# Optimization experiments

Hardware: AMD Instinct MI355X
Metric: run time of the kernel (lower is better)

The kernel has to match this reference:

```python
import jax, jax.numpy as jnp
from jax import lax
import numpy as np

N, L, LQ, D, AF, K = 4096, 512, 32, 30, 10, 4  # n_sents, sent_len, q_len, embed_dim, extra feats, conv size


def setup_inputs() -> dict:
    key = jax.random.key(0)
    ks = jax.random.split(key, 10)
    fan_conv = 1.0 / np.sqrt(D * K)
    fan_lin = 1.0 / np.sqrt(AF + 3)
    return {
        "sents_embeds": jax.random.normal(ks[0], (N, L, D), jnp.float32),
        "question_embeds": jax.random.normal(ks[1], (LQ, D), jnp.float32),
        "sents_gaf": jax.random.normal(ks[2], (N, AF), jnp.float32),
        "sents_labels": jax.random.randint(ks[3], (N,), 0, 2),
        "conv1_w": jax.random.uniform(ks[4], (D, D, K), jnp.float32, -fan_conv, fan_conv),
        "conv1_b": jax.random.uniform(ks[5], (D,), jnp.float32, -fan_conv, fan_conv),
        "conv2_w": jax.random.uniform(ks[6], (D, D, K), jnp.float32, -fan_conv, fan_conv),
        "conv2_b": jax.random.uniform(ks[7], (D,), jnp.float32, -fan_conv, fan_conv),
        "lin_w": jax.random.uniform(ks[8], (2, AF + 3), jnp.float32, -fan_lin, fan_lin),
        "lin_b": jax.random.uniform(ks[9], (2,), jnp.float32, -fan_lin, fan_lin),
    }


def _conv1d(x, w, b):
    # x: [B, C, T], w: [O, I, K] (torch layout), padding = K-1 both sides (as torch padding=K-1)
    y = lax.conv_general_dilated(x, w, window_strides=(1,), padding=[(K - 1, K - 1)],
                                 dimension_numbers=("NCW", "OIW", "NCW"))
    return y + b[None, :, None]


def _window_pool(x):
    # avg_pool1d(kernel=K, stride=1) over last axis
    return lax.reduce_window(x, 0.0, lax.add, (1, 1, K), (1, 1, 1), "VALID") / K


def _gpool(x):
    # global average pool over last axis -> [B, C]
    return jnp.mean(x, axis=-1)


def _cos(a, b):
    # a: [N, D] or [D], b: [N, D] or [D] -> cosine similarity, broadcasting
    num = jnp.sum(a * b, axis=-1)
    den = jnp.linalg.norm(a, axis=-1) * jnp.linalg.norm(b, axis=-1)
    return num / den


def _forward(sents_embeds, question_embeds, sents_gaf, sents_labels,
             conv1_w, conv1_b, conv2_w, conv2_b, lin_w, lin_b):
    q = question_embeds.T[None]                # [1, D, LQ]
    s = jnp.transpose(sents_embeds, (0, 2, 1))  # [N, D, L]

    # question side (identical every loop iteration in the original)
    q_raw = _gpool(q)[0]                        # [D]
    q1c = _conv1d(q, conv1_w, conv1_b)          # [1, D, LQ+3]
    q1g = _gpool(q1c)[0]                        # [D]
    q1w = _window_pool(q1c)                     # [1, D, LQ]
    q2c = _conv1d(q1w, conv2_w, conv2_b)        # [1, D, LQ+3]
    q2g = _gpool(q2c)[0]                        # [D]

    # sentence side, batched over N
    s_raw = _gpool(s)                           # [N, D]
    s1c = _conv1d(s, conv1_w, conv1_b)          # [N, D, L+3]
    s1g = _gpool(s1c)                           # [N, D]
    s1w = _window_pool(s1c)                     # [N, D, L]
    s2c = _conv1d(s1w, conv2_w, conv2_b)        # [N, D, L+3]
    s2g = _gpool(s2c)                           # [N, D]

    # sim1: original overwrites quest_global_pool in the loop, so i=0 uses the raw
    # question pool and i>0 use the conv2-level question pool from the prior iter.
    sim1_raw = _cos(q_raw[None], s_raw)         # [N]
    sim1_q2 = _cos(q2g[None], s_raw)            # [N]
    sim1 = jnp.where(jnp.arange(s_raw.shape[0]) == 0, sim1_raw, sim1_q2)
    sim2 = _cos(q1g[None], s1g)                 # [N]
    sim3 = _cos(q2g[None], s2g)                 # [N]

    mlp_in = jnp.concatenate([sim1[:, None], sim2[:, None], sim3[:, None], sents_gaf], axis=-1)  # [N, 13]
    logits = mlp_in @ lin_w.T + lin_b           # [N, 2]
    logp = jax.nn.log_softmax(logits, axis=-1)
    cost = -jnp.mean(jnp.take_along_axis(logp, sents_labels[:, None], axis=-1)[:, 0])
    emit = jax.nn.softmax(logp, axis=-1)[:, 1]  # softmax applied to log_softmax, as in original
    return cost, emit


def reference(sents_embeds, question_embeds, sents_gaf, sents_labels,
              conv1_w, conv1_b, conv2_w, conv2_b, lin_w, lin_b):
    return _forward(sents_embeds, question_embeds, sents_gaf, sents_labels,
                    conv1_w, conv1_b, conv2_w, conv2_b, lin_w, lin_b)
```

## Files before the change

### kernel.cpp

```cpp
#include <hip/hip_runtime.h>
#include <math.h>

#define NS 4096
#define LL 512
#define LQS 32
#define DD 30
#define AFN 10
#define KW 4

enum {
  QRAW = 0,
  Q1G  = 30,
  Q2G  = 60,
  NRM  = 90,
  WS1  = 96,
  WS2  = 996,
  OA0  = 1896,
  OA1  = 2796,
  OA2  = 3696,
  OB0  = 4596,
  OB1  = 5496,
  OB2  = 6396,
  WTOT = 7296
};

__global__ __launch_bounds__(256) void prep_kernel(
    const float* __restrict__ qe,
    const float* __restrict__ w1,
    const float* __restrict__ b1,
    const float* __restrict__ w2,
    const float* __restrict__ b2,
    float* __restrict__ ws,
    float* __restrict__ out)
{
    __shared__ float w1s[DD * DD * KW];
    __shared__ float w2s[DD * DD * KW];
    __shared__ float qT[DD][LQS];
    __shared__ float q1c[DD][LQS + 3];
    __shared__ float q1w[DD][LQS];
    __shared__ float q2c[DD][LQS + 3];
    __shared__ float qpool[3][DD];
    const int tid = threadIdx.x;

    for (int f = tid; f < DD * DD * KW; f += 256) {
        w1s[f] = w1[f];
        w2s[f] = w2[f];
    }
    for (int f = tid; f < LQS * DD; f += 256) {
        qT[f % DD][f / DD] = qe[f];
    }
    __syncthreads();

    for (int idx = tid; idx < DD * (LQS + 3); idx += 256) {
        int o = idx / (LQS + 3), t = idx % (LQS + 3);
        float acc = b1[o];
        for (int i = 0; i < DD; i++) {
            const float* w = w1s + (o * DD + i) * KW;
            #pragma unroll
            for (int k = 0; k < KW; k++) {
                int j = t + k - 3;
                if (j >= 0 && j < LQS) acc += qT[i][j] * w[k];
            }
        }
        q1c[o][t] = acc;
    }
    __syncthreads();

    for (int idx = tid; idx < DD * LQS; idx += 256) {
        int o = idx / LQS, t = idx % LQS;
        q1w[o][t] = 0.25f * (q1c[o][t] + q1c[o][t + 1] + q1c[o][t + 2] + q1c[o][t + 3]);
    }
    __syncthreads();

    for (int idx = tid; idx < DD * (LQS + 3); idx += 256) {
        int o = idx / (LQS + 3), t = idx % (LQS + 3);
        float acc = b2[o];
        for (int i = 0; i < DD; i++) {
            const float* w = w2s + (o * DD + i) * KW;
            #pragma unroll
            for (int k = 0; k < KW; k++) {
                int j = t + k - 3;
                if (j >= 0 && j < LQS) acc += q1w[i][j] * w[k];
            }
        }
        q2c[o][t] = acc;
    }
    __syncthreads();

    if (tid < DD) {
        float a = 0.f;
        for (int t = 0; t < LQS; t++) a += qT[tid][t];
        qpool[0][tid] = a * (1.0f / LQS);
        float g1 = 0.f;
        for (int t = 0; t < LQS + 3; t++) g1 += q1c[tid][t];
        qpool[1][tid] = g1 * (1.0f / (LQS + 3));
        float g2 = 0.f;
        for (int t = 0; t < LQS + 3; t++) g2 += q2c[tid][t];
        qpool[2][tid] = g2 * (1.0f / (LQS + 3));
        ws[QRAW + tid] = qpool[0][tid];
        ws[Q1G + tid]  = qpool[1][tid];
        ws[Q2G + tid]  = qpool[2][tid];
    }
    __syncthreads();
    if (tid < 3) {
        float s = 0.f;
        for (int i = 0; i < DD; i++) { float v = qpool[tid][i]; s += v * v; }
        ws[NRM + tid] = sqrtf(s);
    }
    if (tid >= 3 && tid < 6) ws[NRM + tid] = 0.f;
    if (tid == 0) out[0] = 0.0f;

    for (int idx = tid; idx < DD * DD; idx += 256) {
        int o = idx / DD, i = idx % DD;
        int tr = i * DD + o;
        const float* w = w1s + idx * KW;
        float a = w[0], b = w[1], c = w[2], d = w[3];
        ws[WS1 + tr] = a + b + c + d;
        ws[OA0 + tr] = 3.f * d + 2.f * c + b;
        ws[OA1 + tr] = 2.f * d + c;
        ws[OA2 + tr] = d;
        ws[OB0 + tr] = a;
        ws[OB1 + tr] = b + 2.f * a;
        ws[OB2 + tr] = c + 2.f * b + 3.f * a;
        const float* v = w2s + idx * KW;
        ws[WS2 + tr] = v[0] + v[1] + v[2] + v[3];
    }
}

__global__ __launch_bounds__(256) void stream_post_kernel(
    const float* __restrict__ se,
    const float* __restrict__ gaf,
    const int*   __restrict__ labels,
    const float* __restrict__ b1,
    const float* __restrict__ b2,
    const float* __restrict__ linw,
    const float* __restrict__ linb,
    const float* __restrict__ ws,
    float* __restrict__ out)
{
    const int n   = blockIdx.x;
    const int tid = threadIdx.x;
    const float* base = se + (size_t)n * (LL * DD);

    __shared__ float tabs[WTOT];
    __shared__ float partial[960];
    __shared__ float bnd[6][DD];

    {
        const float4* src = (const float4*)ws;
        float4* dst = (float4*)tabs;
        #pragma unroll
        for (int f = tid; f < WTOT / 4; f += 256) dst[f] = src[f];
    }
    if (tid < 240) {
        const float4* p = (const float4*)base + tid;
        float sx = 0.f, sy = 0.f, sz = 0.f, sw = 0.f;
        #pragma unroll
        for (int it = 0; it < 16; it++) {
            float4 v = p[it * 240];
            sx += v.x; sy += v.y; sz += v.z; sw += v.w;
        }
        partial[4 * tid + 0] = sx;
        partial[4 * tid + 1] = sy;
        partial[4 * tid + 2] = sz;
        partial[4 * tid + 3] = sw;
    }
    if (tid < 180) {
        int r = tid / DD, c = tid % DD;
        int j = (r < 3) ? r : (LL - 6 + r);
        bnd[r][c] = base[j * DD + c];
    }
    __syncthreads();

    if (tid < 64) {
        const int lane = tid;
        const bool act = (lane < DD);
        const int  ic  = act ? lane : 0;

        float S_i = 0.f;
        #pragma unroll
        for (int m = 0; m < 32; m++) S_i += partial[ic + DD * m];

        float e0r = bnd[0][ic], e1r = bnd[1][ic], e2r = bnd[2][ic];
        float e3r = bnd[3][ic], e4r = bnd[4][ic], e5r = bnd[5][ic];
        float bb1 = b1[ic], bb2 = b2[ic];

        float dotS = 0.f, edge = 0.f;
        #pragma unroll 6
        for (int ii = 0; ii < DD; ii++) {
            float s   = __shfl(S_i, ii, 64);
            float b0  = __shfl(e0r, ii, 64);
            float b1v = __shfl(e1r, ii, 64);
            float b2v = __shfl(e2r, ii, 64);
            float b3v = __shfl(e3r, ii, 64);
            float b4v = __shfl(e4r, ii, 64);
            float b5v = __shfl(e5r, ii, 64);
            const int t = ii * DD + ic;
            dotS += s * tabs[WS1 + t];
            edge += b0 * tabs[OA0 + t] + b1v * tabs[OA1 + t] + b2v * tabs[OA2 + t]
                  + b3v * tabs[OB0 + t] + b4v * tabs[OB1 + t] + b5v * tabs[OB2 + t];
        }
        float s1g = dotS * (1.0f / (LL + 3)) + bb1;
        float Tv  = dotS + (float)LL * bb1 - 0.25f * edge;

        float dot2 = 0.f;
        #pragma unroll 6
        for (int ii = 0; ii < DD; ii++) {
            float tv = __shfl(Tv, ii, 64);
            dot2 += tv * tabs[WS2 + ii * DD + ic];
        }
        float s2g = dot2 * (1.0f / (LL + 3)) + bb2;

        float qv = (n == 0) ? tabs[QRAW + ic] : tabs[Q2G + ic];
        float q1 = tabs[Q1G + ic];
        float q2 = tabs[Q2G + ic];
        float p0 = act ? qv * S_i : 0.f;
        float p1 = act ? S_i * S_i : 0.f;
        float p2 = act ? q1 * s1g : 0.f;
        float p3 = act ? s1g * s1g : 0.f;
        float p4 = act ? q2 * s2g : 0.f;
        float p5 = act ? s2g * s2g : 0.f;
        #pragma unroll
        for (int off = 32; off >= 1; off >>= 1) {
            p0 += __shfl_xor(p0, off, 64);
            p1 += __shfl_xor(p1, off, 64);
            p2 += __shfl_xor(p2, off, 64);
            p3 += __shfl_xor(p3, off, 64);
            p4 += __shfl_xor(p4, off, 64);
            p5 += __shfl_xor(p5, off, 64);
        }

        if (lane == 0) {
            float nq = (n == 0) ? tabs[NRM + 0] : tabs[NRM + 2];
            float sim1 = p0 / (nq * sqrtf(p1));
            float sim2 = p2 / (tabs[NRM + 1] * sqrtf(p3));
            float sim3 = p4 / (tabs[NRM + 2] * sqrtf(p5));

            float in[3 + AFN];
            in[0] = sim1; in[1] = sim2; in[2] = sim3;
            const float* g = gaf + (size_t)n * AFN;
            #pragma unroll
            for (int j = 0; j < AFN; j++) in[3 + j] = g[j];

            float l0 = linb[0], l1 = linb[1];
            #pragma unroll
            for (int j = 0; j < 3 + AFN; j++) {
                l0 += in[j] * linw[j];
                l1 += in[j] * linw[(3 + AFN) + j];
            }
            float m = fmaxf(l0, l1);
            float lse = m + logf(expf(l0 - m) + expf(l1 - m));
            float lp0 = l0 - lse, lp1 = l1 - lse;
            float mm = fmaxf(lp0, lp1);
            float ee0 = expf(lp0 - mm), ee1 = expf(lp1 - mm);
            out[1 + n] = ee1 / (ee0 + ee1);
            int lab = labels[n];
            float lp = (lab == 0) ? lp0 : lp1;
            atomicAdd(&out[0], -lp * (1.0f / NS));
        }
    }
}

extern "C" void kernel_launch(void* const* d_in, const int* in_sizes, int n_in,
                              void* d_out, int out_size, void* d_ws, size_t ws_size,
                              hipStream_t stream)
{
    (void)in_sizes; (void)n_in; (void)out_size; (void)ws_size;
    const float* se  = (const float*)d_in[0];
    const float* qe  = (const float*)d_in[1];
    const float* gaf = (const float*)d_in[2];
    const int*   lab = (const int*)d_in[3];
    const float* w1  = (const float*)d_in[4];
    const float* b1  = (const float*)d_in[5];
    const float* w2  = (const float*)d_in[6];
    const float* b2  = (const float*)d_in[7];
    const float* lw  = (const float*)d_in[8];
    const float* lb  = (const float*)d_in[9];
    float* out = (float*)d_out;
    float* ws  = (float*)d_ws;

    hipLaunchKernelGGL(prep_kernel, dim3(1), dim3(256), 0, stream,
                       qe, w1, b1, w2, b2, ws, out);
    hipLaunchKernelGGL(stream_post_kernel, dim3(NS), dim3(256), 0, stream,
                       se, gaf, lab, b1, b2, lw, lb, ws, out);
}
```

Baseline: 425.4 us.

## Process four sentences per block with double-buffered prefetch of next sentence

```diff
diff --git a/kernel.cpp b/kernel.cpp
--- a/kernel.cpp
+++ b/kernel.cpp
@@ -7,6 +7,8 @@
 #define DD 30
 #define AFN 10
 #define KW 4
+#define SPB 4
+#define NBLK (NS / SPB)
 
 enum {
   QRAW = 0,
@@ -138,126 +140,175 @@
     const float* __restrict__ ws,
     float* __restrict__ out)
 {
-    const int n   = blockIdx.x;
     const int tid = threadIdx.x;
-    const float* base = se + (size_t)n * (LL * DD);
+    const int n0  = blockIdx.x * SPB;
 
     __shared__ float tabs[WTOT];
-    __shared__ float partial[960];
-    __shared__ float bnd[6][DD];
+    __shared__ float partial[2][960];
+    __shared__ float bnd[2][6][DD];
 
     {
         const float4* src = (const float4*)ws;
         float4* dst = (float4*)tabs;
-        #pragma unroll
         for (int f = tid; f < WTOT / 4; f += 256) dst[f] = src[f];
     }
-    if (tid < 240) {
-        const float4* p = (const float4*)base + tid;
-        float sx = 0.f, sy = 0.f, sz = 0.f, sw = 0.f;
-        #pragma unroll
-        for (int it = 0; it < 16; it++) {
-            float4 v = p[it * 240];
-            sx += v.x; sy += v.y; sz += v.z; sw += v.w;
-        }
-        partial[4 * tid + 0] = sx;
-        partial[4 * tid + 1] = sy;
-        partial[4 * tid + 2] = sz;
-        partial[4 * tid + 3] = sw;
-    }
-    if (tid < 180) {
-        int r = tid / DD, c = tid % DD;
-        int j = (r < 3) ? r : (LL - 6 + r);
-        bnd[r][c] = base[j * DD + c];
-    }
-    __syncthreads();
-
-    if (tid < 64) {
-        const int lane = tid;
-        const bool act = (lane < DD);
-        const int  ic  = act ? lane : 0;
-
-        float S_i = 0.f;
-        #pragma unroll
-        for (int m = 0; m < 32; m++) S_i += partial[ic + DD * m];
-
-        float e0r = bnd[0][ic], e1r = bnd[1][ic], e2r = bnd[2][ic];
-        float e3r = bnd[3][ic], e4r = bnd[4][ic], e5r = bnd[5][ic];
-        float bb1 = b1[ic], bb2 = b2[ic];
-
-        float dotS = 0.f, edge = 0.f;
-        #pragma unroll 6
-        for (int ii = 0; ii < DD; ii++) {
-            float s   = __shfl(S_i, ii, 64);
-            float b0  = __shfl(e0r, ii, 64);
-            float b1v = __shfl(e1r, ii, 64);
-            float b2v = __shfl(e2r, ii, 64);
-            float b3v = __shfl(e3r, ii, 64);
-            float b4v = __shfl(e4r, ii, 64);
-            float b5v = __shfl(e5r, ii, 64);
-            const int t = ii * DD + ic;
-            dotS += s * tabs[WS1 + t];
-            edge += b0 * tabs[OA0 + t] + b1v * tabs[OA1 + t] + b2v * tabs[OA2 + t]
-                  + b3v * tabs[OB0 + t] + b4v * tabs[OB1 + t] + b5v * tabs[OB2 + t];
-        }
-        float s1g = dotS * (1.0f / (LL + 3)) + bb1;
-        float Tv  = dotS + (float)LL * bb1 - 0.25f * edge;
-
-        float dot2 = 0.f;
-        #pragma unroll 6
-        for (int ii = 0; ii < DD; ii++) {
-            float tv = __shfl(Tv, ii, 64);
-            dot2 += tv * tabs[WS2 + ii * DD + ic];
-        }
-        float s2g = dot2 * (1.0f / (LL + 3)) + bb2;
-
-        float qv = (n == 0) ? tabs[QRAW + ic] : tabs[Q2G + ic];
-        float q1 = tabs[Q1G + ic];
-        float q2 = tabs[Q2G + ic];
-        float p0 = act ? qv * S_i : 0.f;
-        float p1 = act ? S_i * S_i : 0.f;
-        float p2 = act ? q1 * s1g : 0.f;
-        float p3 = act ? s1g * s1g : 0.f;
-        float p4 = act ? q2 * s2g : 0.f;
-        float p5 = act ? s2g * s2g : 0.f;
-        #pragma unroll
-        for (int off = 32; off >= 1; off >>= 1) {
-            p0 += __shfl_xor(p0, off, 64);
-            p1 += __shfl_xor(p1, off, 64);
-            p2 += __shfl_xor(p2, off, 64);
-            p3 += __shfl_xor(p3, off, 64);
-            p4 += __shfl_xor(p4, off, 64);
-            p5 += __shfl_xor(p5, off, 64);
-        }
-
-        if (lane == 0) {
-            float nq = (n == 0) ? tabs[NRM + 0] : tabs[NRM + 2];
-            float sim1 = p0 / (nq * sqrtf(p1));
-            float sim2 = p2 / (tabs[NRM + 1] * sqrtf(p3));
-            float sim3 = p4 / (tabs[NRM + 2] * sqrtf(p5));
-
-            float in[3 + AFN];
-            in[0] = sim1; in[1] = sim2; in[2] = sim3;
-            const float* g = gaf + (size_t)n * AFN;
-            #pragma unroll
-            for (int j = 0; j < AFN; j++) in[3 + j] = g[j];
-
-            float l0 = linb[0], l1 = linb[1];
-            #pragma unroll
-            for (int j = 0; j < 3 + AFN; j++) {
-                l0 += in[j] * linw[j];
-                l1 += in[j] * linw[(3 + AFN) + j];
-            }
-            float m = fmaxf(l0, l1);
-            float lse = m + logf(expf(l0 - m) + expf(l1 - m));
-            float lp0 = l0 - lse, lp1 = l1 - lse;
-            float mm = fmaxf(lp0, lp1);
-            float ee0 = expf(lp0 - mm), ee1 = expf(lp1 - mm);
-            out[1 + n] = ee1 / (ee0 + ee1);
-            int lab = labels[n];
-            float lp = (lab == 0) ? lp0 : lp1;
-            atomicAdd(&out[0], -lp * (1.0f / NS));
-        }
+
+    {
+        const float* base = se + (size_t)n0 * (LL * DD);
+        if (tid < 240) {
+            const float4* p = (const float4*)base + tid;
+            float sx = 0.f, sy = 0.f, sz = 0.f, sw = 0.f;
+            #pragma unroll
+            for (int it = 0; it < 16; it++) {
+                float4 v = p[it * 240];
+                sx += v.x; sy += v.y; sz += v.z; sw += v.w;
+            }
+            partial[0][4 * tid + 0] = sx;
+            partial[0][4 * tid + 1] = sy;
+            partial[0][4 * tid + 2] = sz;
+            partial[0][4 * tid + 3] = sw;
+        }
+        if (tid < 180) {
+            int r = tid / DD, c = tid % DD;
+            int j = (r < 3) ? r : (LL - 6 + r);
+            bnd[0][r][c] = base[j * DD + c];
+        }
+    }
+    __syncthreads();
+
+    for (int s = 0; s < SPB; s++) {
+        const int cur = s & 1, nxt = cur ^ 1;
+        const bool hn = (s + 1 < SPB);
+        const float* nbase = se + (size_t)(n0 + s + 1) * (LL * DD);
+
+        float4 v0, v1, v2, v3, v4, v5, v6, v7;
+        float bv = 0.f;
+        if (hn && tid < 240) {
+            const float4* p = (const float4*)nbase + tid;
+            v0 = p[0 * 240]; v1 = p[1 * 240]; v2 = p[2 * 240]; v3 = p[3 * 240];
+            v4 = p[4 * 240]; v5 = p[5 * 240]; v6 = p[6 * 240]; v7 = p[7 * 240];
+        }
+        if (hn && tid < 180) {
+            int r = tid / DD, c = tid % DD;
+            int j = (r < 3) ? r : (LL - 6 + r);
+            bv = nbase[j * DD + c];
+        }
+
+        if (tid < 64) {
+            const int n   = n0 + s;
+            const int lane = tid;
+            const bool act = (lane < DD);
+            const int  ic  = act ? lane : 0;
+
+            float S_i = 0.f;
+            #pragma unroll
+            for (int m = 0; m < 32; m++) S_i += partial[cur][ic + DD * m];
+
+            float e0r = bnd[cur][0][ic], e1r = bnd[cur][1][ic], e2r = bnd[cur][2][ic];
+            float e3r = bnd[cur][3][ic], e4r = bnd[cur][4][ic], e5r = bnd[cur][5][ic];
+            float bb1 = b1[ic], bb2 = b2[ic];
+
+            float dotS = 0.f, edge = 0.f;
+            #pragma unroll 6
+            for (int ii = 0; ii < DD; ii++) {
+                float sv  = __shfl(S_i, ii, 64);
+                float b0  = __shfl(e0r, ii, 64);
+                float b1v = __shfl(e1r, ii, 64);
+                float b2v = __shfl(e2r, ii, 64);
+                float b3v = __shfl(e3r, ii, 64);
+                float b4v = __shfl(e4r, ii, 64);
+                float b5v = __shfl(e5r, ii, 64);
+                const int t = ii * DD + ic;
+                dotS += sv * tabs[WS1 + t];
+                edge += b0 * tabs[OA0 + t] + b1v * tabs[OA1 + t] + b2v * tabs[OA2 + t]
+                      + b3v * tabs[OB0 + t] + b4v * tabs[OB1 + t] + b5v * tabs[OB2 + t];
+            }
+            float s1g = dotS * (1.0f / (LL + 3)) + bb1;
+            float Tv  = dotS + (float)LL * bb1 - 0.25f * edge;
+
+            float dot2 = 0.f;
+            #pragma unroll 6
+            for (int ii = 0; ii < DD; ii++) {
+                float tv = __shfl(Tv, ii, 64);
+                dot2 += tv * tabs[WS2 + ii * DD + ic];
+            }
+            float s2g = dot2 * (1.0f / (LL + 3)) + bb2;
+
+            float qv = (n == 0) ? tabs[QRAW + ic] : tabs[Q2G + ic];
+            float q1 = tabs[Q1G + ic];
+            float q2 = tabs[Q2G + ic];
+            float p0 = act ? qv * S_i : 0.f;
+            float p1 = act ? S_i * S_i : 0.f;
+            float p2 = act ? q1 * s1g : 0.f;
+            float p3 = act ? s1g * s1g : 0.f;
+            float p4 = act ? q2 * s2g : 0.f;
+            float p5 = act ? s2g * s2g : 0.f;
+            #pragma unroll
+            for (int off = 32; off >= 1; off >>= 1) {
+                p0 += __shfl_xor(p0, off, 64);
+                p1 += __shfl_xor(p1, off, 64);
+                p2 += __shfl_xor(p2, off, 64);
+                p3 += __shfl_xor(p3, off, 64);
+                p4 += __shfl_xor(p4, off, 64);
+                p5 += __shfl_xor(p5, off, 64);
+            }
+
+            if (lane == 0) {
+                float nq = (n == 0) ? tabs[NRM + 0] : tabs[NRM + 2];
+                float sim1 = p0 / (nq * sqrtf(p1));
+                float sim2 = p2 / (tabs[NRM + 1] * sqrtf(p3));
+                float sim3 = p4 / (tabs[NRM + 2] * sqrtf(p5));
+
+                float in[3 + AFN];
+                in[0] = sim1; in[1] = sim2; in[2] = sim3;
+                const float* g = gaf + (size_t)n * AFN;
+                #pragma unroll
+                for (int j = 0; j < AFN; j++) in[3 + j] = g[j];
+
+                float l0 = linb[0], l1 = linb[1];
+                #pragma unroll
+                for (int j = 0; j < 3 + AFN; j++) {
+                    l0 += in[j] * linw[j];
+                    l1 += in[j] * linw[(3 + AFN) + j];
+                }
+                float m = fmaxf(l0, l1);
+                float lse = m + logf(expf(l0 - m) + expf(l1 - m));
+                float lp0 = l0 - lse, lp1 = l1 - lse;
+                float mm = fmaxf(lp0, lp1);
+                float ee0 = expf(lp0 - mm), ee1 = expf(lp1 - mm);
+                out[1 + n] = ee1 / (ee0 + ee1);
+                int lab = labels[n];
+                float lp = (lab == 0) ? lp0 : lp1;
+                atomicAdd(&out[0], -lp * (1.0f / NS));
+            }
+        }
+
+        if (hn && tid < 240) {
+            const float4* p = (const float4*)nbase + tid;
+            float sx = 0.f, sy = 0.f, sz = 0.f, sw = 0.f;
+            sx += v0.x; sy += v0.y; sz += v0.z; sw += v0.w;
+            sx += v1.x; sy += v1.y; sz += v1.z; sw += v1.w;
+            sx += v2.x; sy += v2.y; sz += v2.z; sw += v2.w;
+            sx += v3.x; sy += v3.y; sz += v3.z; sw += v3.w;
+            sx += v4.x; sy += v4.y; sz += v4.z; sw += v4.w;
+            sx += v5.x; sy += v5.y; sz += v5.z; sw += v5.w;
+            sx += v6.x; sy += v6.y; sz += v6.z; sw += v6.w;
+            sx += v7.x; sy += v7.y; sz += v7.z; sw += v7.w;
+            #pragma unroll
+            for (int it = 8; it < 16; it++) {
+                float4 u = p[it * 240];
+                sx += u.x; sy += u.y; sz += u.z; sw += u.w;
+            }
+            partial[nxt][4 * tid + 0] = sx;
+            partial[nxt][4 * tid + 1] = sy;
+            partial[nxt][4 * tid + 2] = sz;
+            partial[nxt][4 * tid + 3] = sw;
+        }
+        if (hn && tid < 180) {
+            int r = tid / DD, c = tid % DD;
+            bnd[nxt][r][c] = bv;
+        }
+        __syncthreads();
     }
 }
 
@@ -281,6 +332,6 @@
 
     hipLaunchKernelGGL(prep_kernel, dim3(1), dim3(256), 0, stream,
                        qe, w1, b1, w2, b2, ws, out);
-    hipLaunchKernelGGL(stream_post_kernel, dim3(NS), dim3(256), 0, stream,
+    hipLaunchKernelGGL(stream_post_kernel, dim3(NBLK), dim3(256), 0, stream,
                        se, gaf, lab, b1, b2, lw, lb, ws, out);
 }
```

New measurement: 427.2 us. No clear change (+0.4%).
